# Optimization experiments

Hardware: AMD Instinct MI355X
Metric: run time of the kernel (lower is better)

Reference implementation:

```python
import jax, jax.numpy as jnp
import numpy as np

E = 8      # number of experts (sublayers)
N = 8192   # tokens / batch rows
D = 1024   # sublayer input size (max_sublayer_input_size)
H = 2048   # sublayer output size
O = 1024   # output_encoding_size


def setup_inputs() -> dict:
    key = jax.random.key(0)
    k0, k1, k2, k3 = jax.random.split(key, 4)
    x_feat = jax.random.normal(k0, (N, D), dtype=jnp.float32)
    expert_idx = jax.random.randint(k1, (N,), 0, E)  # exclusive (top-1) routing
    # Stacked expert params: sublayers = Linear(D,H), encoders = Linear(H,O)
    W1 = jax.random.normal(k2, (E, D, H), dtype=jnp.float32) * (1.0 / np.sqrt(D))
    b1 = jnp.zeros((E, H), dtype=jnp.float32)
    W2 = jax.random.normal(k3, (E, H, O), dtype=jnp.float32) * (1.0 / np.sqrt(H))
    b2 = jnp.zeros((E, O), dtype=jnp.float32)
    return {"x_feat": x_feat, "W1": W1, "b1": b1, "W2": W2, "b2": b2,
            "expert_idx": expert_idx}


def reference(x_feat, W1, b1, W2, b2, expert_idx):
    # one-hot sublayer_mask (last E columns of the original x)
    onehot = jax.nn.one_hot(expert_idx, E, dtype=x_feat.dtype)  # [N, E]
    # Exclusive dispatch: each token goes through exactly one expert.
    # Structural loop over the fixed E experts; combine via the one-hot mask
    # (equivalent to the original gather -> sublayer -> encoder -> scatter).
    enc = jnp.zeros((x_feat.shape[0], O), dtype=x_feat.dtype)
    for i in range(E):
        h = x_feat @ W1[i] + b1[i]          # [N, H] sublayer
        y = h @ W2[i] + b2[i]               # [N, O] encoder
        enc = enc + onehot[:, i:i + 1] * y  # keep only rows routed to expert i
    # output = [encoded (O cols) | sublayer_mask (E cols)]
    return jnp.concatenate([enc, onehot], axis=1)
```

## Files before the change

kernel.cpp:

```cpp
#include <hip/hip_runtime.h>

#define NTOK 8192
#define DDIM 1024
#define HDIM 2048
#define ODIM 1024
#define NEXP 8
#define OUTW (ODIM + NEXP)
#define MT_MAX 64

typedef __bf16 bf16_t;
typedef bf16_t bf16x8 __attribute__((ext_vector_type(8)));
typedef bf16_t bf16x4 __attribute__((ext_vector_type(4)));
typedef float f32x4 __attribute__((ext_vector_type(4)));

__device__ __forceinline__ void gld_lds16(bf16_t* lds, const bf16_t* g) {
  __builtin_amdgcn_global_load_lds(
      (__attribute__((address_space(1))) void*)g,
      (__attribute__((address_space(3))) void*)lds, 16, 0, 0);
}

__global__ void zero_cnt_kernel(int* cnt) {
  if (threadIdx.x < NEXP) cnt[threadIdx.x] = 0;
}

__global__ void route_kernel(const int* __restrict__ idx, float* __restrict__ out,
                             int* __restrict__ rank, int* cnt) {
  __shared__ int lcnt[NEXP];
  __shared__ int lbase[NEXP];
  int t = threadIdx.x;
  if (t < NEXP) lcnt[t] = 0;
  __syncthreads();
  int n = blockIdx.x * 256 + t;
  int e = idx[n];
  int lr = atomicAdd(&lcnt[e], 1);
  __syncthreads();
  if (t < NEXP) lbase[t] = atomicAdd(&cnt[t], lcnt[t]);
  __syncthreads();
  rank[n] = lbase[e] + lr;
  float* o = out + (size_t)n * OUTW + ODIM;
#pragma unroll
  for (int j = 0; j < NEXP; j++) o[j] = (j == e) ? 1.0f : 0.0f;
}

__global__ void scan_kernel(const int* __restrict__ cnt, int* __restrict__ off) {
  if (threadIdx.x == 0) {
    int s = 0;
    for (int e = 0; e < NEXP; e++) { off[e] = s; s += cnt[e]; }
  }
}

__global__ void gather_kernel(const float* __restrict__ x, const int* __restrict__ idx,
                              const int* __restrict__ rank, const int* __restrict__ off,
                              bf16_t* __restrict__ xg, int* __restrict__ tok_of_pos) {
  int n = blockIdx.x;
  int e = idx[n];
  int pos = off[e] + rank[n];
  if (threadIdx.x == 0) tok_of_pos[pos] = n;
  float4 v = ((const float4*)(x + (size_t)n * DDIM))[threadIdx.x];
  bf16x4 o;
  o[0] = (bf16_t)v.x; o[1] = (bf16_t)v.y; o[2] = (bf16_t)v.z; o[3] = (bf16_t)v.w;
  *(bf16x4*)(xg + (size_t)pos * DDIM + threadIdx.x * 4) = o;
}

__global__ __launch_bounds__(256) void wtrans_kernel(const float* __restrict__ src,
                                                     bf16_t* __restrict__ dst,
                                                     int R, int C) {
  __shared__ float t[128][65];
  int e = blockIdx.z;
  int c0 = blockIdx.x * 64, r0g = blockIdx.y * 128;
  int tid = threadIdx.x;
  const float* s = src + (size_t)e * R * C;
#pragma unroll
  for (int p = 0; p < 8; p++) {
    int r = (tid >> 4) + p * 16;
    int c4 = (tid & 15) * 4;
    float4 v = *(const float4*)&s[(size_t)(r0g + r) * C + c0 + c4];
    t[r][c4 + 0] = v.x;
    t[r][c4 + 1] = v.y;
    t[r][c4 + 2] = v.z;
    t[r][c4 + 3] = v.w;
  }
  __syncthreads();
  bf16_t* d = dst + (size_t)e * R * C;
  int w = tid >> 6, l = tid & 63;
#pragma unroll
  for (int itc = 0; itc < 2; itc++) {
#pragma unroll
    for (int it2 = 0; it2 < 2; it2++) {
      int c = (l >> 3) + 8 * w + 32 * itc;
      int r0 = (l & 7) * 8 + 64 * it2;
      bf16x8 o;
#pragma unroll
      for (int j = 0; j < 8; j++) o[j] = (bf16_t)t[r0 + j][c];
      *(bf16x8*)&d[(size_t)(c0 + c) * R + r0g + r0] = o;
    }
  }
}

template <int KDIM, int NCOLS, int MTG, bool TO_BF16>
__global__ __launch_bounds__(256) void gemm_kernel(
    const bf16_t* __restrict__ A, const bf16_t* __restrict__ Bt,
    const float* __restrict__ bias,
    const int* __restrict__ cnt, const int* __restrict__ off,
    const int* __restrict__ tok_of_pos,
    bf16_t* __restrict__ outb, float* __restrict__ outf) {
  constexpr int NT = NCOLS / 128;
  const int b = blockIdx.x;
  const int e = b & 7;
  int t = b >> 3;
  const int mtl = t % MTG;
  t /= MTG;
  const int nt = t % NT;
  const int g = t / NT;
  const int mt = g * MTG + mtl;

  const int count = cnt[e];
  if (mt * 128 >= count) return;
  const int base = off[e];

  __shared__ bf16_t lA[128 * 32];
  __shared__ bf16_t lB[128 * 32];

  const int tid = threadIdx.x;
  const int lane = tid & 63;
  const int wave = tid >> 6;
  const int mrow = lane & 15;
  const int q = lane >> 4;
  const int wm = (wave & 1) * 64;
  const int wn = (wave >> 1) * 64;

  const bf16_t* pA[2];
  const bf16_t* pB[2];
#pragma unroll
  for (int s = 0; s < 2; s++) {
    int lrow = wave * 32 + s * 16 + (lane >> 2);
    int kq = (lane & 3) ^ (lrow & 3);
    int gr = base + mt * 128 + lrow;
    if (gr > NTOK - 1) gr = NTOK - 1;
    pA[s] = A + (size_t)gr * KDIM + kq * 8;
    int nrow = nt * 128 + lrow;
    pB[s] = Bt + ((size_t)e * NCOLS + nrow) * KDIM + kq * 8;
  }

  f32x4 acc[4][4] = {};
  const bf16_t* la0 = &lA[(wm + mrow) * 32 + ((q ^ (mrow & 3)) * 8)];
  const bf16_t* lb0 = &lB[(wn + mrow) * 32 + ((q ^ (mrow & 3)) * 8)];

  for (int kk = 0; kk < KDIM; kk += 32) {
#pragma unroll
    for (int s = 0; s < 2; s++) {
      gld_lds16(&lA[(wave * 2 + s) * 512], pA[s] + kk);
      gld_lds16(&lB[(wave * 2 + s) * 512], pB[s] + kk);
    }
    __syncthreads();
    bf16x8 af[4], bfr[4];
#pragma unroll
    for (int i = 0; i < 4; i++) {
      af[i]  = *(const bf16x8*)(la0 + i * 16 * 32);
      bfr[i] = *(const bf16x8*)(lb0 + i * 16 * 32);
    }
#pragma unroll
    for (int i = 0; i < 4; i++)
#pragma unroll
      for (int j = 0; j < 4; j++)
        acc[i][j] = __builtin_amdgcn_mfma_f32_16x16x32_bf16(af[i], bfr[j], acc[i][j], 0, 0, 0);
    __syncthreads();
  }

  const int mlimit = count - mt * 128;
  float bs[4];
#pragma unroll
  for (int j = 0; j < 4; j++)
    bs[j] = bias[(size_t)e * NCOLS + nt * 128 + wn + j * 16 + mrow];

#pragma unroll
  for (int i = 0; i < 4; i++) {
#pragma unroll
    for (int r = 0; r < 4; r++) {
      int ml = wm + i * 16 + q * 4 + r;
      if (ml < mlimit) {
        int prow = base + mt * 128 + ml;
        if constexpr (TO_BF16) {
          bf16_t* orow = outb + (size_t)prow * NCOLS;
#pragma unroll
          for (int j = 0; j < 4; j++)
            orow[nt * 128 + wn + j * 16 + mrow] = (bf16_t)(acc[i][j][r] + bs[j]);
        } else {
          int tok = tok_of_pos[prow];
          float* orow = outf + (size_t)tok * OUTW;
#pragma unroll
          for (int j = 0; j < 4; j++)
            orow[nt * 128 + wn + j * 16 + mrow] = acc[i][j][r] + bs[j];
        }
      }
    }
  }
}

extern "C" void kernel_launch(void* const* d_in, const int* in_sizes, int n_in,
                              void* d_out, int out_size, void* d_ws, size_t ws_size,
                              hipStream_t stream) {
  const float* x  = (const float*)d_in[0];
  const float* W1 = (const float*)d_in[1];
  const float* b1 = (const float*)d_in[2];
  const float* W2 = (const float*)d_in[3];
  const float* b2 = (const float*)d_in[4];
  const int* idx  = (const int*)d_in[5];
  float* out = (float*)d_out;

  char* ws = (char*)d_ws;
  bf16_t* xg  = (bf16_t*)(ws);
  bf16_t* hg  = (bf16_t*)(ws + 16777216);
  bf16_t* Wt1 = (bf16_t*)(ws + 50331648);
  bf16_t* Wt2 = (bf16_t*)(ws + 83886080);
  int* tok    = (int*)(ws + 117440512);
  int* rank   = (int*)(ws + 117473280);
  int* cnt    = (int*)(ws + 117506048);
  int* off    = (int*)(ws + 117506080);

  zero_cnt_kernel<<<1, 64, 0, stream>>>(cnt);
  route_kernel<<<NTOK / 256, 256, 0, stream>>>(idx, out, rank, cnt);
  scan_kernel<<<1, 64, 0, stream>>>(cnt, off);
  gather_kernel<<<NTOK, 256, 0, stream>>>(x, idx, rank, off, xg, tok);
  wtrans_kernel<<<dim3(HDIM / 64, DDIM / 128, NEXP), 256, 0, stream>>>(W1, Wt1, DDIM, HDIM);
  wtrans_kernel<<<dim3(ODIM / 64, HDIM / 128, NEXP), 256, 0, stream>>>(W2, Wt2, HDIM, ODIM);
  gemm_kernel<DDIM, HDIM, 8, true>
      <<<NEXP * MT_MAX * (HDIM / 128), 256, 0, stream>>>(
      xg, Wt1, b1, cnt, off, tok, hg, nullptr);
  gemm_kernel<HDIM, ODIM, 4, false>
      <<<NEXP * MT_MAX * (ODIM / 128), 256, 0, stream>>>(
      hg, Wt2, b2, cnt, off, tok, nullptr, out);
}
```

Before: 314.5 us.

## Deepen GEMM K-tile to 64, merge weight transposes, gather one row per wave

The GEMM's K step per iteration grows from 32 to 64, and the LDS layout gets an 8-way XOR swizzle. This halves the number of barrier pairs and load batches per output tile. The two weight-transpose launches are merged into a single 1D launch that picks W1 or W2 by block index, and the gather kernel now processes four tokens per block with one wave per row. LDS use per block doubles, which may affect occupancy, and the loop is still single-buffered.

After: 328.2 us. +4.3%, slower.

```diff
diff --git a/kernel.cpp b/kernel.cpp
--- a/kernel.cpp
+++ b/kernel.cpp
@@ -49,25 +49,38 @@
   }
 }
 
-__global__ void gather_kernel(const float* __restrict__ x, const int* __restrict__ idx,
-                              const int* __restrict__ rank, const int* __restrict__ off,
-                              bf16_t* __restrict__ xg, int* __restrict__ tok_of_pos) {
-  int n = blockIdx.x;
+__global__ __launch_bounds__(256) void gather_kernel(
+    const float* __restrict__ x, const int* __restrict__ idx,
+    const int* __restrict__ rank, const int* __restrict__ off,
+    bf16_t* __restrict__ xg, int* __restrict__ tok_of_pos) {
+  int wave = threadIdx.x >> 6, lane = threadIdx.x & 63;
+  int n = blockIdx.x * 4 + wave;
   int e = idx[n];
   int pos = off[e] + rank[n];
-  if (threadIdx.x == 0) tok_of_pos[pos] = n;
-  float4 v = ((const float4*)(x + (size_t)n * DDIM))[threadIdx.x];
-  bf16x4 o;
-  o[0] = (bf16_t)v.x; o[1] = (bf16_t)v.y; o[2] = (bf16_t)v.z; o[3] = (bf16_t)v.w;
-  *(bf16x4*)(xg + (size_t)pos * DDIM + threadIdx.x * 4) = o;
-}
-
-__global__ __launch_bounds__(256) void wtrans_kernel(const float* __restrict__ src,
-                                                     bf16_t* __restrict__ dst,
-                                                     int R, int C) {
+  if (lane == 0) tok_of_pos[pos] = n;
+  const float4* xr = (const float4*)(x + (size_t)n * DDIM);
+  bf16x4* og = (bf16x4*)(xg + (size_t)pos * DDIM);
+#pragma unroll
+  for (int r = 0; r < 4; r++) {
+    float4 v = xr[lane + r * 64];
+    bf16x4 o;
+    o[0] = (bf16_t)v.x; o[1] = (bf16_t)v.y; o[2] = (bf16_t)v.z; o[3] = (bf16_t)v.w;
+    og[lane + r * 64] = o;
+  }
+}
+
+__global__ __launch_bounds__(256) void wtrans_kernel(
+    const float* __restrict__ W1s, bf16_t* __restrict__ W1d,
+    const float* __restrict__ W2s, bf16_t* __restrict__ W2d) {
   __shared__ float t[128][65];
-  int e = blockIdx.z;
-  int c0 = blockIdx.x * 64, r0g = blockIdx.y * 128;
+  int id = blockIdx.x;
+  const float* src; bf16_t* dst; int R, C, tid2;
+  if (id < 2048) { src = W1s; dst = W1d; R = DDIM; C = HDIM; tid2 = id; }
+  else           { src = W2s; dst = W2d; R = HDIM; C = ODIM; tid2 = id - 2048; }
+  int ntc = C / 64;
+  int e = tid2 / (ntc * (R / 128));
+  int rem = tid2 % (ntc * (R / 128));
+  int c0 = (rem % ntc) * 64, r0g = (rem / ntc) * 128;
   int tid = threadIdx.x;
   const float* s = src + (size_t)e * R * C;
 #pragma unroll
@@ -118,8 +131,8 @@
   if (mt * 128 >= count) return;
   const int base = off[e];
 
-  __shared__ bf16_t lA[128 * 32];
-  __shared__ bf16_t lB[128 * 32];
+  __shared__ bf16_t lA[128 * 64];
+  __shared__ bf16_t lB[128 * 64];
 
   const int tid = threadIdx.x;
   const int lane = tid & 63;
@@ -129,41 +142,48 @@
   const int wm = (wave & 1) * 64;
   const int wn = (wave >> 1) * 64;
 
-  const bf16_t* pA[2];
-  const bf16_t* pB[2];
-#pragma unroll
-  for (int s = 0; s < 2; s++) {
-    int lrow = wave * 32 + s * 16 + (lane >> 2);
-    int kq = (lane & 3) ^ (lrow & 3);
+  const bf16_t* pA[4];
+  const bf16_t* pB[4];
+  const int gchunk = (lane & 7) ^ (lane >> 3);
+#pragma unroll
+  for (int s = 0; s < 4; s++) {
+    int lrow = (wave * 4 + s) * 8 + (lane >> 3);
     int gr = base + mt * 128 + lrow;
     if (gr > NTOK - 1) gr = NTOK - 1;
-    pA[s] = A + (size_t)gr * KDIM + kq * 8;
+    pA[s] = A + (size_t)gr * KDIM + gchunk * 8;
     int nrow = nt * 128 + lrow;
-    pB[s] = Bt + ((size_t)e * NCOLS + nrow) * KDIM + kq * 8;
+    pB[s] = Bt + ((size_t)e * NCOLS + nrow) * KDIM + gchunk * 8;
   }
 
   f32x4 acc[4][4] = {};
-  const bf16_t* la0 = &lA[(wm + mrow) * 32 + ((q ^ (mrow & 3)) * 8)];
-  const bf16_t* lb0 = &lB[(wn + mrow) * 32 + ((q ^ (mrow & 3)) * 8)];
-
-  for (int kk = 0; kk < KDIM; kk += 32) {
-#pragma unroll
-    for (int s = 0; s < 2; s++) {
-      gld_lds16(&lA[(wave * 2 + s) * 512], pA[s] + kk);
-      gld_lds16(&lB[(wave * 2 + s) * 512], pB[s] + kk);
+  const int xr = mrow & 7;
+  const bf16_t* la0 = &lA[(wm + mrow) * 64];
+  const bf16_t* lb0 = &lB[(wn + mrow) * 64];
+  const int o0 = (q ^ xr) * 8;
+  const int o1 = ((4 + q) ^ xr) * 8;
+
+  for (int kk = 0; kk < KDIM; kk += 64) {
+#pragma unroll
+    for (int s = 0; s < 4; s++) {
+      gld_lds16(&lA[(wave * 4 + s) * 512], pA[s] + kk);
+      gld_lds16(&lB[(wave * 4 + s) * 512], pB[s] + kk);
     }
     __syncthreads();
-    bf16x8 af[4], bfr[4];
-#pragma unroll
-    for (int i = 0; i < 4; i++) {
-      af[i]  = *(const bf16x8*)(la0 + i * 16 * 32);
-      bfr[i] = *(const bf16x8*)(lb0 + i * 16 * 32);
-    }
-#pragma unroll
-    for (int i = 0; i < 4; i++)
-#pragma unroll
-      for (int j = 0; j < 4; j++)
-        acc[i][j] = __builtin_amdgcn_mfma_f32_16x16x32_bf16(af[i], bfr[j], acc[i][j], 0, 0, 0);
+#pragma unroll
+    for (int ks = 0; ks < 2; ks++) {
+      const int o = ks ? o1 : o0;
+      bf16x8 af[4], bfr[4];
+#pragma unroll
+      for (int i = 0; i < 4; i++) {
+        af[i]  = *(const bf16x8*)(la0 + i * 16 * 64 + o);
+        bfr[i] = *(const bf16x8*)(lb0 + i * 16 * 64 + o);
+      }
+#pragma unroll
+      for (int i = 0; i < 4; i++)
+#pragma unroll
+        for (int j = 0; j < 4; j++)
+          acc[i][j] = __builtin_amdgcn_mfma_f32_16x16x32_bf16(af[i], bfr[j], acc[i][j], 0, 0, 0);
+    }
     __syncthreads();
   }
 
@@ -221,9 +241,8 @@
   zero_cnt_kernel<<<1, 64, 0, stream>>>(cnt);
   route_kernel<<<NTOK / 256, 256, 0, stream>>>(idx, out, rank, cnt);
   scan_kernel<<<1, 64, 0, stream>>>(cnt, off);
-  gather_kernel<<<NTOK, 256, 0, stream>>>(x, idx, rank, off, xg, tok);
-  wtrans_kernel<<<dim3(HDIM / 64, DDIM / 128, NEXP), 256, 0, stream>>>(W1, Wt1, DDIM, HDIM);
-  wtrans_kernel<<<dim3(ODIM / 64, HDIM / 128, NEXP), 256, 0, stream>>>(W2, Wt2, HDIM, ODIM);
+  gather_kernel<<<NTOK / 4, 256, 0, stream>>>(x, idx, rank, off, xg, tok);
+  wtrans_kernel<<<4096, 256, 0, stream>>>(W1, Wt1, W2, Wt2);
   gemm_kernel<DDIM, HDIM, 8, true>
       <<<NEXP * MT_MAX * (HDIM / 128), 256, 0, stream>>>(
       xg, Wt1, b1, cnt, off, tok, hg, nullptr);
```
